# Kernel tuning notes

Hardware: AMD Instinct MI355X
Metric: run time of the kernel (lower is better)

The kernel has to match this reference:

```python
import jax, jax.numpy as jnp
import numpy as np


def _build_transform():
    # Deterministic re-creation of SegmentationAugmentation.build_3d_transform
    # with flip=True, offset=0.1, scale=0.2, rotate=True.
    rng = np.random.default_rng(0)
    t = np.eye(4, dtype=np.float32)
    for i in range(3):
        if rng.random() > 0.5:
            t[i, i] *= -1.0
        t[i, 3] = 0.1 * (rng.random() * 2.0 - 1.0)
        t[i, i] *= 1.0 + 0.2 * (rng.random() * 2.0 - 1.0)
    a = rng.random() * 2.0 * np.pi
    s, c = np.sin(a), np.cos(a)
    rot = np.array([[c, -s, 0, 0], [s, c, 0, 0], [0, 0, 1, 0], [0, 0, 0, 1]],
                   dtype=np.float32)
    return t @ rot


def _affine_grid(theta, size):
    # theta: [B,3,4]; size: (B,C,D,H,W); align_corners=False.
    B, C, D, H, W = size
    def lin(n):
        # pixel-center normalized coords: (2i+1)/n - 1
        return (2.0 * jnp.arange(n, dtype=jnp.float32) + 1.0) / n - 1.0
    z, y, x = jnp.meshgrid(lin(D), lin(H), lin(W), indexing='ij')
    pts = jnp.stack([x, y, z], axis=-1)  # [D,H,W,3], (x,y,z) order as in torch
    return (jnp.einsum('bij,dhwj->bdhwi', theta[:, :, :3], pts)
            + theta[:, None, None, None, :, 3])


def _grid_sample_3d_border(inp, grid):
    # trilinear grid_sample, padding_mode='border', align_corners=False.
    # inp: [B,C,D,H,W]; grid: [B,Do,Ho,Wo,3] with (x,y,z) normalized coords.
    B, C, D, H, W = inp.shape
    Do, Ho, Wo = grid.shape[1:4]

    def unnorm(cn, n):
        # align_corners=False unnormalize, then border clamp
        return jnp.clip(((cn + 1.0) * n - 1.0) * 0.5, 0.0, n - 1.0)

    x = unnorm(grid[..., 0], W)
    y = unnorm(grid[..., 1], H)
    z = unnorm(grid[..., 2], D)
    x0 = jnp.floor(x); y0 = jnp.floor(y); z0 = jnp.floor(z)
    fx, fy, fz = x - x0, y - y0, z - z0
    x0i = x0.astype(jnp.int32); y0i = y0.astype(jnp.int32); z0i = z0.astype(jnp.int32)
    x1i = jnp.minimum(x0i + 1, W - 1)
    y1i = jnp.minimum(y0i + 1, H - 1)
    z1i = jnp.minimum(z0i + 1, D - 1)

    inp_flat = inp.reshape(B, C, D * H * W)
    N = Do * Ho * Wo
    out = jnp.zeros((B, C, N), dtype=inp.dtype)
    for zi, wz in ((z0i, 1.0 - fz), (z1i, fz)):
        for yi, wy in ((y0i, 1.0 - fy), (y1i, fy)):
            for xi, wx in ((x0i, 1.0 - fx), (x1i, fx)):
                idx = ((zi * H + yi) * W + xi).reshape(B, 1, N)
                v = jnp.take_along_axis(
                    inp_flat, jnp.broadcast_to(idx, (B, C, N)), axis=2)
                w = (wz * wy * wx).reshape(B, 1, N)
                out = out + v * w
    return out.reshape(B, C, Do, Ho, Wo)


def setup_inputs() -> dict:
    key = jax.random.key(0)
    k1, k2 = jax.random.split(key)
    input_g = jax.random.normal(k1, (8, 1, 128, 128, 128), dtype=jnp.float32)
    label_g = jax.random.uniform(k2, (8, 1, 128, 128, 128), dtype=jnp.float32)
    transform = jnp.asarray(_build_transform())
    return {"input_g": input_g, "label_g": label_g, "transform": transform}


def reference(input_g, label_g, transform):
    # transpose(-3,-1): swap depth and width axes
    inp = jnp.swapaxes(input_g, -3, -1)
    lab = jnp.swapaxes(label_g, -3, -1)
    B = inp.shape[0]
    theta = jnp.broadcast_to(transform[:3][None], (B, 3, 4)).astype(jnp.float32)
    grid = _affine_grid(theta, inp.shape)
    aug_inp = _grid_sample_3d_border(inp, grid)
    aug_lab = _grid_sample_3d_border(lab, grid)
    aug_inp = jnp.swapaxes(aug_inp, -3, -1)
    aug_lab = jnp.swapaxes(aug_lab, -3, -1)
    return aug_inp, aug_lab > 0.5
```

## Files before the change

kernel.cpp:

```cpp
#include <hip/hip_runtime.h>


#define NV 128
#define TOTAL (8 * NV * NV * NV)

typedef float v2f __attribute__((ext_vector_type(2)));

__global__ __launch_bounds__(128) void seg_aug_kernel(
    const float* __restrict__ in,
    const float* __restrict__ lab,
    const float* __restrict__ T,
    float* __restrict__ out_in,
    float* __restrict__ out_lab)
{
#pragma clang fp contract(off)
    __shared__ __align__(16) float s[4 * NV * 2 + 2];

    const int t  = threadIdx.x;
    const int o3 = blockIdx.x & (NV - 1);
    const int o2 = (blockIdx.x >> 7) & (NV - 1);
    const int b  = blockIdx.x >> 14;

    float p2 = (2.0f * (float)o2 + 1.0f) / 128.0f - 1.0f;
    float p3 = (2.0f * (float)o3 + 1.0f) / 128.0f - 1.0f;
    float ux = (T[0] * p2 + T[1] * p3) + T[3];
    float uy = (T[4] * p2 + T[5] * p3) + T[7];
    float gx = ((ux + 1.0f) * 128.0f - 1.0f) * 0.5f;
    float gy = ((uy + 1.0f) * 128.0f - 1.0f) * 0.5f;
    gx = fminf(fmaxf(gx, 0.0f), 127.0f);
    gy = fminf(fmaxf(gy, 0.0f), 127.0f);
    float fx0f = floorf(gx), fy0f = floorf(gy);
    float fx = gx - fx0f;
    float fy = gy - fy0f;
    const int ix0 = __builtin_amdgcn_readfirstlane((int)fx0f);
    const int iy0 = __builtin_amdgcn_readfirstlane((int)fy0f);
    const int ix1 = min(ix0 + 1, NV - 1);
    const int iy1 = min(iy0 + 1, NV - 1);
    float wx0 = 1.0f - fx, wx1 = fx;
    float wy0 = 1.0f - fy, wy1 = fy;

    const size_t bbase = (size_t)b << 21;
    const int rid = t >> 5;
    const int seg = t & 31;
    const int ixS = (rid & 2) ? ix1 : ix0;
    const int iyS = (rid & 1) ? iy1 : iy0;
    const int goff = (ixS * NV + iyS) * NV + seg * 4;
    const float4 i4 = *(const float4*)(in  + bbase + goff);
    const float4 l4 = *(const float4*)(lab + bbase + goff);

    float p4 = (2.0f * (float)t + 1.0f) / 128.0f - 1.0f;
    float uz = T[10] * p4 + T[11];
    float gz = ((uz + 1.0f) * 128.0f - 1.0f) * 0.5f;
    gz = fminf(fmaxf(gz, 0.0f), 127.0f);
    float fz0f = floorf(gz);
    float fz = gz - fz0f;
    const int iz0 = (int)fz0f;
    float wz0 = 1.0f - fz, wz1 = fz;

    if (t < 2) s[4 * NV * 2 + t] = 0.0f;

    {
        float* d = &s[(rid * NV + seg * 4) * 2];
        ((float4*)d)[0] = make_float4(i4.x, l4.x, i4.y, l4.y);
        ((float4*)d)[1] = make_float4(i4.z, l4.z, i4.w, l4.w);
    }
    __syncthreads();

    const v2f* srow = (const v2f*)s;
    v2f a0 = srow[0 * NV + iz0], b0 = srow[0 * NV + iz0 + 1];
    v2f a1 = srow[1 * NV + iz0], b1 = srow[1 * NV + iz0 + 1];
    v2f a2 = srow[2 * NV + iz0], b2 = srow[2 * NV + iz0 + 1];
    v2f a3 = srow[3 * NV + iz0], b3 = srow[3 * NV + iz0 + 1];

    float tz0y0 = wz0 * wy0, tz0y1 = wz0 * wy1;
    float tz1y0 = wz1 * wy0, tz1y1 = wz1 * wy1;
    float w1 = tz0y0 * wx0, w2 = tz0y0 * wx1;
    float w3 = tz0y1 * wx0, w4 = tz0y1 * wx1;
    float w5 = tz1y0 * wx0, w6 = tz1y0 * wx1;
    float w7 = tz1y1 * wx0, w8 = tz1y1 * wx1;

    v2f acc = {0.0f, 0.0f};
    acc = acc + a0 * w1;
    acc = acc + a2 * w2;
    acc = acc + a1 * w3;
    acc = acc + a3 * w4;
    acc = acc + b0 * w5;
    acc = acc + b2 * w6;
    acc = acc + b1 * w7;
    acc = acc + b3 * w8;

    const int oidx = blockIdx.x * NV + t;
    out_in[oidx]  = acc.x;
    out_lab[oidx] = (acc.y > 0.5f) ? 1.0f : 0.0f;
}

extern "C" void kernel_launch(void* const* d_in, const int* in_sizes, int n_in,
                              void* d_out, int out_size, void* d_ws, size_t ws_size,
                              hipStream_t stream) {
    const float* in  = (const float*)d_in[0];
    const float* lab = (const float*)d_in[1];
    const float* T   = (const float*)d_in[2];
    float* out_in  = (float*)d_out;
    float* out_lab = (float*)d_out + TOTAL;

    dim3 grid(TOTAL / 128);
    dim3 block(128);
    seg_aug_kernel<<<grid, block, 0, stream>>>(in, lab, T, out_in, out_lab);
}
```

Measured before the change: 246.1 us.

## Pipeline per-wave column processing with async global-to-LDS double buffering

Reworks the kernel so that each 64-lane wave handles a chunk of 32 output columns. Global reads of the four source rows go straight to LDS through global_load_lds into a double-buffered per-wave area, and the next column's loads are issued before the current column is computed, with vmcnt waits and no block-wide barriers. Each lane now produces two outputs and writes them as a nontemporal 2-wide store. This is meant to hide memory latency and cut per-block launch and sync overhead, but it relies on hand-tuned waitcnt counts and on the assumption that LDS writes from loads to LDS are visible to the wave without a barrier.

```diff
diff --git a/kernel.cpp b/kernel.cpp
--- a/kernel.cpp
+++ b/kernel.cpp
@@ -3,10 +3,14 @@
 
 #define NV 128
 #define TOTAL (8 * NV * NV * NV)
+#define WPB 8
+#define WSTRIDE 1032
+#define CHUNK 32
+#define NBLK (TOTAL / NV / WPB / CHUNK)
 
 typedef float v2f __attribute__((ext_vector_type(2)));
 
-__global__ __launch_bounds__(128) void seg_aug_kernel(
+__global__ __launch_bounds__(512, 4) void seg_aug_kernel(
     const float* __restrict__ in,
     const float* __restrict__ lab,
     const float* __restrict__ T,
@@ -14,84 +18,191 @@
     float* __restrict__ out_lab)
 {
 #pragma clang fp contract(off)
-    __shared__ __align__(16) float s[4 * NV * 2 + 2];
-
-    const int t  = threadIdx.x;
-    const int o3 = blockIdx.x & (NV - 1);
-    const int o2 = (blockIdx.x >> 7) & (NV - 1);
-    const int b  = blockIdx.x >> 14;
-
-    float p2 = (2.0f * (float)o2 + 1.0f) / 128.0f - 1.0f;
-    float p3 = (2.0f * (float)o3 + 1.0f) / 128.0f - 1.0f;
-    float ux = (T[0] * p2 + T[1] * p3) + T[3];
-    float uy = (T[4] * p2 + T[5] * p3) + T[7];
-    float gx = ((ux + 1.0f) * 128.0f - 1.0f) * 0.5f;
-    float gy = ((uy + 1.0f) * 128.0f - 1.0f) * 0.5f;
-    gx = fminf(fmaxf(gx, 0.0f), 127.0f);
-    gy = fminf(fmaxf(gy, 0.0f), 127.0f);
-    float fx0f = floorf(gx), fy0f = floorf(gy);
-    float fx = gx - fx0f;
-    float fy = gy - fy0f;
-    const int ix0 = __builtin_amdgcn_readfirstlane((int)fx0f);
-    const int iy0 = __builtin_amdgcn_readfirstlane((int)fy0f);
-    const int ix1 = min(ix0 + 1, NV - 1);
-    const int iy1 = min(iy0 + 1, NV - 1);
-    float wx0 = 1.0f - fx, wx1 = fx;
-    float wy0 = 1.0f - fy, wy1 = fy;
-
+    __shared__ __align__(16) float s[WPB * 2 * WSTRIDE];
+
+    const int t = threadIdx.x;
+    const int l = t & 63;
+    const int w = __builtin_amdgcn_readfirstlane(t >> 6);
+    const int gw = blockIdx.x * WPB + w;
+    const int col0 = gw * CHUNK;
+    const int b = col0 >> 14;
     const size_t bbase = (size_t)b << 21;
-    const int rid = t >> 5;
-    const int seg = t & 31;
-    const int ixS = (rid & 2) ? ix1 : ix0;
-    const int iyS = (rid & 1) ? iy1 : iy0;
-    const int goff = (ixS * NV + iyS) * NV + seg * 4;
-    const float4 i4 = *(const float4*)(in  + bbase + goff);
-    const float4 l4 = *(const float4*)(lab + bbase + goff);
-
-    float p4 = (2.0f * (float)t + 1.0f) / 128.0f - 1.0f;
-    float uz = T[10] * p4 + T[11];
-    float gz = ((uz + 1.0f) * 128.0f - 1.0f) * 0.5f;
-    gz = fminf(fmaxf(gz, 0.0f), 127.0f);
-    float fz0f = floorf(gz);
-    float fz = gz - fz0f;
-    const int iz0 = (int)fz0f;
-    float wz0 = 1.0f - fz, wz1 = fz;
-
-    if (t < 2) s[4 * NV * 2 + t] = 0.0f;
-
-    {
-        float* d = &s[(rid * NV + seg * 4) * 2];
-        ((float4*)d)[0] = make_float4(i4.x, l4.x, i4.y, l4.y);
-        ((float4*)d)[1] = make_float4(i4.z, l4.z, i4.w, l4.w);
+    const float* ibp = in  + bbase;
+    const float* lbp = lab + bbase;
+    float* sw0 = &s[w * 2 * WSTRIDE];
+    float* sw1 = sw0 + WSTRIDE;
+    if (l == 0) { sw0[512] = 0.0f; sw0[1028] = 0.0f;
+                  sw1[512] = 0.0f; sw1[1028] = 0.0f; }
+
+    const float T0 = T[0], T1 = T[1], T3v = T[3];
+    const float T4 = T[4], T5 = T[5], T7v = T[7];
+    const float T10 = T[10], T11 = T[11];
+
+    float p4a = (2.0f * (float)(2 * l) + 1.0f) / 128.0f - 1.0f;
+    float uza = T10 * p4a + T11;
+    float gza = ((uza + 1.0f) * 128.0f - 1.0f) * 0.5f;
+    gza = fminf(fmaxf(gza, 0.0f), 127.0f);
+    float fz0a = floorf(gza);
+    const int   iza = (int)fz0a;
+    const float fza = gza - fz0a;
+    float p4b = (2.0f * (float)(2 * l + 1) + 1.0f) / 128.0f - 1.0f;
+    float uzb = T10 * p4b + T11;
+    float gzb = ((uzb + 1.0f) * 128.0f - 1.0f) * 0.5f;
+    gzb = fminf(fmaxf(gzb, 0.0f), 127.0f);
+    float fz0b = floorf(gzb);
+    const int   izb = (int)fz0b;
+    const float fzb = gzb - fz0b;
+    const float awz0 = 1.0f - fza, awz1 = fza;
+    const float bwz0 = 1.0f - fzb, bwz1 = fzb;
+
+    const int segoff = (l & 31) * 4;
+    const bool loA = (l < 32);
+
+    #define STAGE(COL, SW, FXV, FYV)                                          \
+    {                                                                         \
+        const int o3 = (COL) & (NV - 1);                                      \
+        const int o2 = ((COL) >> 7) & (NV - 1);                               \
+        float p2 = (2.0f * (float)o2 + 1.0f) / 128.0f - 1.0f;                 \
+        float p3 = (2.0f * (float)o3 + 1.0f) / 128.0f - 1.0f;                 \
+        float ux = (T0 * p2 + T1 * p3) + T3v;                                 \
+        float uy = (T4 * p2 + T5 * p3) + T7v;                                 \
+        float gx = ((ux + 1.0f) * 128.0f - 1.0f) * 0.5f;                      \
+        float gy = ((uy + 1.0f) * 128.0f - 1.0f) * 0.5f;                      \
+        gx = fminf(fmaxf(gx, 0.0f), 127.0f);                                  \
+        gy = fminf(fmaxf(gy, 0.0f), 127.0f);                                  \
+        float fx0f = floorf(gx), fy0f = floorf(gy);                           \
+        FXV = gx - fx0f;                                                      \
+        FYV = gy - fy0f;                                                      \
+        const int ix0 = __builtin_amdgcn_readfirstlane((int)fx0f);            \
+        const int iy0 = __builtin_amdgcn_readfirstlane((int)fy0f);            \
+        const int ix1 = min(ix0 + 1, NV - 1);                                 \
+        const int iy1 = min(iy0 + 1, NV - 1);                                 \
+        const int r00 = (ix0 * NV + iy0) * NV;                                \
+        const int r01 = (ix0 * NV + iy1) * NV;                                \
+        const int r10 = (ix1 * NV + iy0) * NV;                                \
+        const int r11 = (ix1 * NV + iy1) * NV;                                \
+        const int offA = (loA ? r00 : r01) + segoff;                          \
+        const int offB = (loA ? r10 : r11) + segoff;                          \
+        __builtin_amdgcn_global_load_lds(ibp + offA, (SW),       16, 0, 0);   \
+        __builtin_amdgcn_global_load_lds(ibp + offB, (SW) + 256, 16, 0, 0);   \
+        __builtin_amdgcn_global_load_lds(lbp + offA, (SW) + 516, 16, 0, 0);   \
+        __builtin_amdgcn_global_load_lds(lbp + offB, (SW) + 772, 16, 0, 0);   \
     }
-    __syncthreads();
-
-    const v2f* srow = (const v2f*)s;
-    v2f a0 = srow[0 * NV + iz0], b0 = srow[0 * NV + iz0 + 1];
-    v2f a1 = srow[1 * NV + iz0], b1 = srow[1 * NV + iz0 + 1];
-    v2f a2 = srow[2 * NV + iz0], b2 = srow[2 * NV + iz0 + 1];
-    v2f a3 = srow[3 * NV + iz0], b3 = srow[3 * NV + iz0 + 1];
-
-    float tz0y0 = wz0 * wy0, tz0y1 = wz0 * wy1;
-    float tz1y0 = wz1 * wy0, tz1y1 = wz1 * wy1;
-    float w1 = tz0y0 * wx0, w2 = tz0y0 * wx1;
-    float w3 = tz0y1 * wx0, w4 = tz0y1 * wx1;
-    float w5 = tz1y0 * wx0, w6 = tz1y0 * wx1;
-    float w7 = tz1y1 * wx0, w8 = tz1y1 * wx1;
-
-    v2f acc = {0.0f, 0.0f};
-    acc = acc + a0 * w1;
-    acc = acc + a2 * w2;
-    acc = acc + a1 * w3;
-    acc = acc + a3 * w4;
-    acc = acc + b0 * w5;
-    acc = acc + b2 * w6;
-    acc = acc + b1 * w7;
-    acc = acc + b3 * w8;
-
-    const int oidx = blockIdx.x * NV + t;
-    out_in[oidx]  = acc.x;
-    out_lab[oidx] = (acc.y > 0.5f) ? 1.0f : 0.0f;
+
+    #define COMPUTE(COL, SW, FXV, FYV)                                        \
+    {                                                                         \
+        const float wx0 = 1.0f - (FXV), wx1 = (FXV);                          \
+        const float wy0 = 1.0f - (FYV), wy1 = (FYV);                          \
+        float atz0y0 = awz0 * wy0, atz0y1 = awz0 * wy1;                       \
+        float atz1y0 = awz1 * wy0, atz1y1 = awz1 * wy1;                       \
+        float aw1 = atz0y0 * wx0, aw2 = atz0y0 * wx1;                         \
+        float aw3 = atz0y1 * wx0, aw4 = atz0y1 * wx1;                         \
+        float aw5 = atz1y0 * wx0, aw6 = atz1y0 * wx1;                         \
+        float aw7 = atz1y1 * wx0, aw8 = atz1y1 * wx1;                         \
+        float btz0y0 = bwz0 * wy0, btz0y1 = bwz0 * wy1;                       \
+        float btz1y0 = bwz1 * wy0, btz1y1 = bwz1 * wy1;                       \
+        float bw1 = btz0y0 * wx0, bw2 = btz0y0 * wx1;                         \
+        float bw3 = btz0y1 * wx0, bw4 = btz0y1 * wx1;                         \
+        float bw5 = btz1y0 * wx0, bw6 = btz1y0 * wx1;                         \
+        float bw7 = btz1y1 * wx0, bw8 = btz1y1 * wx1;                         \
+        const int obase = (COL) * NV;                                         \
+        {                                                                     \
+            const float* rpa = (SW) + iza;                                    \
+            float a00 = rpa[0*NV], a00p = rpa[0*NV+1];                        \
+            float a01 = rpa[1*NV], a01p = rpa[1*NV+1];                        \
+            float a10 = rpa[2*NV], a10p = rpa[2*NV+1];                        \
+            float a11 = rpa[3*NV], a11p = rpa[3*NV+1];                        \
+            float acc_a = 0.0f;                                               \
+            acc_a = acc_a + a00  * aw1;                                       \
+            acc_a = acc_a + a10  * aw2;                                       \
+            acc_a = acc_a + a01  * aw3;                                       \
+            acc_a = acc_a + a11  * aw4;                                       \
+            acc_a = acc_a + a00p * aw5;                                       \
+            acc_a = acc_a + a10p * aw6;                                       \
+            acc_a = acc_a + a01p * aw7;                                       \
+            acc_a = acc_a + a11p * aw8;                                       \
+            const float* rpb = (SW) + izb;                                    \
+            float c00 = rpb[0*NV], c00p = rpb[0*NV+1];                        \
+            float c01 = rpb[1*NV], c01p = rpb[1*NV+1];                        \
+            float c10 = rpb[2*NV], c10p = rpb[2*NV+1];                        \
+            float c11 = rpb[3*NV], c11p = rpb[3*NV+1];                        \
+            float acc_b = 0.0f;                                               \
+            acc_b = acc_b + c00  * bw1;                                       \
+            acc_b = acc_b + c10  * bw2;                                       \
+            acc_b = acc_b + c01  * bw3;                                       \
+            acc_b = acc_b + c11  * bw4;                                       \
+            acc_b = acc_b + c00p * bw5;                                       \
+            acc_b = acc_b + c10p * bw6;                                       \
+            acc_b = acc_b + c01p * bw7;                                       \
+            acc_b = acc_b + c11p * bw8;                                       \
+            v2f v; v.x = acc_a; v.y = acc_b;                                  \
+            __builtin_nontemporal_store(v, (v2f*)(out_in + obase) + l);       \
+        }                                                                     \
+        {                                                                     \
+            const float* lpa = (SW) + 516 + iza;                              \
+            float a00 = lpa[0*NV], a00p = lpa[0*NV+1];                        \
+            float a01 = lpa[1*NV], a01p = lpa[1*NV+1];                        \
+            float a10 = lpa[2*NV], a10p = lpa[2*NV+1];                        \
+            float a11 = lpa[3*NV], a11p = lpa[3*NV+1];                        \
+            float acc_a = 0.0f;                                               \
+            acc_a = acc_a + a00  * aw1;                                       \
+            acc_a = acc_a + a10  * aw2;                                       \
+            acc_a = acc_a + a01  * aw3;                                       \
+            acc_a = acc_a + a11  * aw4;                                       \
+            acc_a = acc_a + a00p * aw5;                                       \
+            acc_a = acc_a + a10p * aw6;                                       \
+            acc_a = acc_a + a01p * aw7;                                       \
+            acc_a = acc_a + a11p * aw8;                                       \
+            const float* lpb = (SW) + 516 + izb;                              \
+            float c00 = lpb[0*NV], c00p = lpb[0*NV+1];                        \
+            float c01 = lpb[1*NV], c01p = lpb[1*NV+1];                        \
+            float c10 = lpb[2*NV], c10p = lpb[2*NV+1];                        \
+            float c11 = lpb[3*NV], c11p = lpb[3*NV+1];                        \
+            float acc_b = 0.0f;                                               \
+            acc_b = acc_b + c00  * bw1;                                       \
+            acc_b = acc_b + c10  * bw2;                                       \
+            acc_b = acc_b + c01  * bw3;                                       \
+            acc_b = acc_b + c11  * bw4;                                       \
+            acc_b = acc_b + c00p * bw5;                                       \
+            acc_b = acc_b + c10p * bw6;                                       \
+            acc_b = acc_b + c01p * bw7;                                       \
+            acc_b = acc_b + c11p * bw8;                                       \
+            v2f v;                                                            \
+            v.x = (acc_a > 0.5f) ? 1.0f : 0.0f;                               \
+            v.y = (acc_b > 0.5f) ? 1.0f : 0.0f;                               \
+            __builtin_nontemporal_store(v, (v2f*)(out_lab + obase) + l);      \
+        }                                                                     \
+    }
+
+    float fxc, fyc, fxn, fyn;
+    float* cur = sw0;
+    float* nxt = sw1;
+
+    STAGE(col0, cur, fxc, fyc);
+
+    STAGE(col0 + 1, nxt, fxn, fyn);
+    asm volatile("s_waitcnt vmcnt(4)" ::: "memory");
+    __builtin_amdgcn_sched_barrier(0);
+    COMPUTE(col0, cur, fxc, fyc);
+    fxc = fxn; fyc = fyn;
+    { float* tmp = cur; cur = nxt; nxt = tmp; }
+
+#pragma clang loop unroll(disable)
+    for (int k = 1; k <= CHUNK - 2; ++k) {
+        STAGE(col0 + k + 1, nxt, fxn, fyn);
+        asm volatile("s_waitcnt vmcnt(6)" ::: "memory");
+        __builtin_amdgcn_sched_barrier(0);
+        COMPUTE(col0 + k, cur, fxc, fyc);
+        fxc = fxn; fyc = fyn;
+        { float* tmp = cur; cur = nxt; nxt = tmp; }
+    }
+
+    asm volatile("s_waitcnt vmcnt(2)" ::: "memory");
+    __builtin_amdgcn_sched_barrier(0);
+    COMPUTE(col0 + CHUNK - 1, cur, fxc, fyc);
+
+    #undef STAGE
+    #undef COMPUTE
 }
 
 extern "C" void kernel_launch(void* const* d_in, const int* in_sizes, int n_in,
@@ -103,7 +214,6 @@
     float* out_in  = (float*)d_out;
     float* out_lab = (float*)d_out + TOTAL;
 
-    dim3 grid(TOTAL / 128);
-    dim3 block(128);
-    seg_aug_kernel<<<grid, block, 0, stream>>>(in, lab, T, out_in, out_lab);
+    seg_aug_kernel<<<dim3(NBLK), dim3(512), 0, stream>>>(
+        in, lab, T, out_in, out_lab);
 }
```

Result: slower. 264.3 us (+7.4%).
